# Performance work log

Hardware: AMD Instinct MI355X
Metric: run time of the kernel (lower is better)

Reference implementation:

```python
import jax, jax.numpy as jnp
import numpy as np

N = 8192
SOFTENING_LENGTH = 0.01
EPS = SOFTENING_LENGTH ** 2  # softening area, added to squared distances


def setup_inputs() -> dict:
    key = jax.random.key(0)
    k1, k2 = jax.random.split(key)
    y = jax.random.normal(k1, (N, 3), dtype=jnp.float32)
    masses = jax.random.uniform(k2, (N,), dtype=jnp.float32)
    t = jnp.zeros((), dtype=jnp.float32)  # unused by the vector field math
    G = jnp.ones((), dtype=jnp.float32)   # gravitational constant (args=(G,))
    return {"t": t, "y": y, "masses": masses, "G": G}


def reference(t, y, masses, G):
    # Faithful translation of pairwise_gravitational_acceleration with
    # eps = softening_length**2.
    # Original math: acc[j] = sum_i (q[i] - q[j]) * G * masses[j-broadcast]
    #                         * (||q_i - q_j||^2 + eps)^{-3/2}
    # where acc_factors[i, j] = G * masses[j] * inv_dist_cubed[i, j]
    # and the reduction is over axis 0 (i).
    d2 = jnp.sum(y * y, axis=1)                          # [N]
    pairwise_d2 = d2[:, None] + d2[None, :] - 2.0 * (y @ y.T)  # [N, N]
    inv_dist_cubed = (pairwise_d2 + EPS) ** -1.5         # [N, N]
    f = G * masses[None, :] * inv_dist_cubed             # f[i, j]
    # sum_i f[i,j] * (q[i] - q[j]) = (f^T @ q)[j] - q[j] * sum_i f[i,j]
    acc = f.T @ y - y * jnp.sum(f, axis=0)[:, None]      # [N, 3]
    return acc
```

## Files before the change

kernel.cpp:

```cpp
#include <hip/hip_runtime.h>


#define NB 8192
#define TILE 256
constexpr float EPS = 0.01f * 0.01f;

__global__ __launch_bounds__(256) void zero_kernel(float* __restrict__ out, int n) {
    int idx = blockIdx.x * 256 + threadIdx.x;
    if (idx < n) out[idx] = 0.0f;
}

__global__ __launch_bounds__(256) void nbody_kernel(
    const float* __restrict__ y,
    const float* __restrict__ masses,
    const float* __restrict__ Gp,
    float* __restrict__ out)
{
    __shared__ float4 sp[TILE];

    const int tid = threadIdx.x;
    const int j   = blockIdx.x * TILE + tid;
    const int i0  = blockIdx.y * TILE;

    const float xj = y[3 * j + 0];
    const float yj = y[3 * j + 1];
    const float zj = y[3 * j + 2];

    {
        const float* src = y + 3 * i0;
        sp[tid] = make_float4(src[3 * tid + 0], src[3 * tid + 1], src[3 * tid + 2], 0.0f);
    }
    __syncthreads();

    float ax = 0.0f, ay = 0.0f, az = 0.0f;
#pragma unroll 8
    for (int ii = 0; ii < TILE; ++ii) {
        float4 p = sp[ii];
        float dx = p.x - xj;
        float dy = p.y - yj;
        float dz = p.z - zj;
        float r2 = fmaf(dx, dx, fmaf(dy, dy, fmaf(dz, dz, EPS)));
        float rinv  = rsqrtf(r2);
        float rinv3 = rinv * rinv * rinv;
        ax = fmaf(dx, rinv3, ax);
        ay = fmaf(dy, rinv3, ay);
        az = fmaf(dz, rinv3, az);
    }

    const float s = Gp[0] * masses[j];
    atomicAdd(&out[3 * j + 0], ax * s);
    atomicAdd(&out[3 * j + 1], ay * s);
    atomicAdd(&out[3 * j + 2], az * s);
}

extern "C" void kernel_launch(void* const* d_in, const int* in_sizes, int n_in,
                              void* d_out, int out_size, void* d_ws, size_t ws_size,
                              hipStream_t stream) {
    const float* y      = (const float*)d_in[1];
    const float* masses = (const float*)d_in[2];
    const float* Gp     = (const float*)d_in[3];
    float* out = (float*)d_out;

    zero_kernel<<<(3 * NB + 255) / 256, 256, 0, stream>>>(out, 3 * NB);

    dim3 grid(NB / TILE, NB / TILE);
    nbody_kernel<<<grid, 256, 0, stream>>>(y, masses, Gp, out);
}
```

Baseline: 88.95 us.

## Register-block four targets per thread and stream packed sources from global

Each thread now accumulates forces for four target bodies, so every loaded source body is reused across four interactions. Source positions are pre-packed into float4 in workspace and read directly from global memory (uniform, cached broadcast) instead of staged through shared memory with a barrier. The compiler rsqrt builtin replaces rsqrtf. The change adds a pack kernel launch and raises register pressure, and the grid shrinks to 8x64 blocks, which may reduce occupancy on a large GPU.

After: 92.85 us. +4.4%, slower.

```diff
diff --git a/kernel.cpp b/kernel.cpp
--- a/kernel.cpp
+++ b/kernel.cpp
@@ -1,8 +1,11 @@
 #include <hip/hip_runtime.h>
 
 
-#define NB 8192
-#define TILE 256
+#define NB    8192
+#define BLOCK 256
+#define JPT   4
+#define JTILE (BLOCK * JPT)
+#define ITILE 128
 constexpr float EPS = 0.01f * 0.01f;
 
 __global__ __launch_bounds__(256) void zero_kernel(float* __restrict__ out, int n) {
@@ -10,47 +13,61 @@
     if (idx < n) out[idx] = 0.0f;
 }
 
-__global__ __launch_bounds__(256) void nbody_kernel(
-    const float* __restrict__ y,
-    const float* __restrict__ masses,
-    const float* __restrict__ Gp,
+__global__ __launch_bounds__(256) void pack_kernel(const float* __restrict__ y,
+                                                   float4* __restrict__ pack) {
+    int i = blockIdx.x * 256 + threadIdx.x;
+    pack[i] = make_float4(y[3 * i + 0], y[3 * i + 1], y[3 * i + 2], 0.0f);
+}
+
+__global__ __launch_bounds__(BLOCK) void nbody_kernel(
+    const float4* __restrict__ pack,
+    const float*  __restrict__ y,
+    const float*  __restrict__ masses,
+    const float*  __restrict__ Gp,
     float* __restrict__ out)
 {
-    __shared__ float4 sp[TILE];
+    const int tid = threadIdx.x;
+    const int j0  = blockIdx.x * JTILE;
+    const int i0  = blockIdx.y * ITILE;
 
-    const int tid = threadIdx.x;
-    const int j   = blockIdx.x * TILE + tid;
-    const int i0  = blockIdx.y * TILE;
-
-    const float xj = y[3 * j + 0];
-    const float yj = y[3 * j + 1];
-    const float zj = y[3 * j + 2];
-
-    {
-        const float* src = y + 3 * i0;
-        sp[tid] = make_float4(src[3 * tid + 0], src[3 * tid + 1], src[3 * tid + 2], 0.0f);
-    }
-    __syncthreads();
-
-    float ax = 0.0f, ay = 0.0f, az = 0.0f;
-#pragma unroll 8
-    for (int ii = 0; ii < TILE; ++ii) {
-        float4 p = sp[ii];
-        float dx = p.x - xj;
-        float dy = p.y - yj;
-        float dz = p.z - zj;
-        float r2 = fmaf(dx, dx, fmaf(dy, dy, fmaf(dz, dz, EPS)));
-        float rinv  = rsqrtf(r2);
-        float rinv3 = rinv * rinv * rinv;
-        ax = fmaf(dx, rinv3, ax);
-        ay = fmaf(dy, rinv3, ay);
-        az = fmaf(dz, rinv3, az);
+    int   j[JPT];
+    float xj[JPT], yj[JPT], zj[JPT];
+    float ax[JPT], ay[JPT], az[JPT];
+#pragma unroll
+    for (int k = 0; k < JPT; ++k) {
+        int jj = j0 + k * BLOCK + tid;
+        j[k] = jj;
+        xj[k] = y[3 * jj + 0];
+        yj[k] = y[3 * jj + 1];
+        zj[k] = y[3 * jj + 2];
+        ax[k] = ay[k] = az[k] = 0.0f;
     }
 
-    const float s = Gp[0] * masses[j];
-    atomicAdd(&out[3 * j + 0], ax * s);
-    atomicAdd(&out[3 * j + 1], ay * s);
-    atomicAdd(&out[3 * j + 2], az * s);
+#pragma unroll 4
+    for (int ii = 0; ii < ITILE; ++ii) {
+        float4 p = pack[i0 + ii];
+#pragma unroll
+        for (int k = 0; k < JPT; ++k) {
+            float dx = p.x - xj[k];
+            float dy = p.y - yj[k];
+            float dz = p.z - zj[k];
+            float r2 = fmaf(dx, dx, fmaf(dy, dy, fmaf(dz, dz, EPS)));
+            float ri  = __builtin_amdgcn_rsqf(r2);
+            float ri3 = ri * ri * ri;
+            ax[k] = fmaf(dx, ri3, ax[k]);
+            ay[k] = fmaf(dy, ri3, ay[k]);
+            az[k] = fmaf(dz, ri3, az[k]);
+        }
+    }
+
+    const float G = Gp[0];
+#pragma unroll
+    for (int k = 0; k < JPT; ++k) {
+        float s = G * masses[j[k]];
+        atomicAdd(&out[3 * j[k] + 0], ax[k] * s);
+        atomicAdd(&out[3 * j[k] + 1], ay[k] * s);
+        atomicAdd(&out[3 * j[k] + 2], az[k] * s);
+    }
 }
 
 extern "C" void kernel_launch(void* const* d_in, const int* in_sizes, int n_in,
@@ -59,10 +76,12 @@
     const float* y      = (const float*)d_in[1];
     const float* masses = (const float*)d_in[2];
     const float* Gp     = (const float*)d_in[3];
-    float* out = (float*)d_out;
+    float*  out  = (float*)d_out;
+    float4* pack = (float4*)d_ws;
 
     zero_kernel<<<(3 * NB + 255) / 256, 256, 0, stream>>>(out, 3 * NB);
+    pack_kernel<<<NB / 256, 256, 0, stream>>>(y, pack);
 
-    dim3 grid(NB / TILE, NB / TILE);
-    nbody_kernel<<<grid, 256, 0, stream>>>(y, masses, Gp, out);
+    dim3 grid(NB / JTILE, NB / ITILE);
+    nbody_kernel<<<grid, BLOCK, 0, stream>>>(pack, y, masses, Gp, out);
 }
```
